# Optimization experiments

Measured on AMD Instinct MI355X. Metric: run time of the kernel, lower is better.

## Reference

```python
import jax, jax.numpy as jnp
import numpy as np

B, T, E, K, NNEG = 128, 512, 128, 4, 64


def setup_inputs() -> dict:
    key = jax.random.key(0)
    k1, k2, k3, k4 = jax.random.split(key, 4)
    base_payload = jax.random.normal(k1, (B, T, E), dtype=jnp.float32)
    mapped_ctx_payload = jax.random.normal(k2, (B, T, E, K), dtype=jnp.float32)
    seq_lens = jax.random.randint(k3, (B,), 1, T + 1, dtype=jnp.int32)
    # valid positions mask over the flattened (B*T) pool of possible negatives
    valid = (jnp.arange(T)[None, :] < seq_lens[:, None]).reshape(-1)  # [B*T]
    logits = jnp.where(valid, 0.0, -1e30)[None, :]                    # [1, B*T]
    logits = jnp.broadcast_to(logits, (B, B * T))
    # mirrors torch.multinomial(mask, n_negatives): one draw set per batch row
    sample_ids = jax.random.categorical(k4, logits, shape=(NNEG, B)).T.astype(jnp.int32)
    return {
        "base_payload": base_payload,
        "mapped_ctx_payload": mapped_ctx_payload,
        "seq_lens": seq_lens,
        "sample_ids": sample_ids,
    }


def reference(base_payload, mapped_ctx_payload, seq_lens, sample_ids):
    b, t, e = base_payload.shape
    n_steps = mapped_ctx_payload.shape[-1]
    # length mask [b, t]
    len_mask = (jnp.arange(t)[None, :] < seq_lens[:, None]).astype(base_payload.dtype)
    # zero context embeddings past each sequence's length
    trimmed_mce = mapped_ctx_payload * len_mask[:, :, None, None]  # [b, t, e, n_steps]
    # gather sampled negatives from the flattened base embedding pool
    neg_samples = base_payload.reshape(b * t, e)[sample_ids]  # [b, n_neg, e]

    step_losses = []
    for i in range(1, n_steps + 1):
        ce_i = trimmed_mce[:, : t - i, :, i - 1]   # [b, t-i, e]
        be_i = base_payload[:, i:]                  # [b, t-i, e]
        positive_pred = jnp.sum(ce_i * be_i, axis=-1)             # [b, t-i]
        neg_pred = jnp.einsum('bse,bne->bsn', ce_i, neg_samples)  # [b, t-i, n_neg]
        logits = jnp.concatenate([positive_pred[..., None], neg_pred], axis=-1)
        step_losses.append(-jax.nn.log_softmax(logits, axis=-1)[:, :, 0].mean())
    return jnp.stack(step_losses).mean()
```

## Files before the change

kernel.cpp:

```cpp
#include <hip/hip_runtime.h>
#include <math.h>

#define NB 128
#define NT 512
#define NEDIM 128
#define NNEG 64
#define SCHUNK 16
#define NCHUNK (NT / SCHUNK)
#define NBLK (NB * NCHUNK)
#define WSN (NBLK * 4)

typedef __bf16 bf16x8 __attribute__((ext_vector_type(8)));
typedef float  f32x4  __attribute__((ext_vector_type(4)));

__launch_bounds__(256, 4)
__global__ void cpc_mfma_kernel(const float* __restrict__ base,
                                const float* __restrict__ mce,
                                const int*  __restrict__ seq_lens,
                                const int*  __restrict__ sample_ids,
                                float* __restrict__ ws)
{
    const int b    = blockIdx.y;
    const int s0   = blockIdx.x * SCHUNK;
    const int slot = (b * NCHUNK + blockIdx.x) * 4;
    const int L    = seq_lens[b];
    const float LOG65 = 4.1743873f;
    const float wgt[4] = {1.f/261632.f, 1.f/261120.f, 1.f/260608.f, 1.f/260096.f};

    if (s0 >= L) {
        if (threadIdx.x < 4) {
            float c = 0.f;
            #pragma unroll
            for (int i = 1; i <= 4; ++i) {
                int hi = min(SCHUNK, (NT - i) - s0);
                if (hi > 0) c += (float)hi * LOG65 * wgt[i - 1];
            }
            ws[slot + threadIdx.x] = (threadIdx.x == 0) ? c : 0.f;
        }
        return;
    }

    __shared__ __bf16 Afrag[1024 * 8];
    __shared__ __bf16 Bfrag[1536 * 8];

    const int tid  = threadIdx.x;
    const int lane = tid & 63;
    const int w    = tid >> 6;
    const int q    = lane >> 4;
    const int fl   = lane & 15;

    const float4* mce4 = (const float4*)mce;

    {
        int s  = tid & 15;
        int eb = tid >> 4;
        const float4* src = mce4 + (size_t)(b * NT + s0 + s) * NEDIM + eb * 8;
        float4 v[8];
        #pragma unroll
        for (int u = 0; u < 8; ++u) v[u] = src[u];
        const float* vf = (const float*)v;
        int Cs = (eb >> 2) * 4 + (s >> 2);
        int base_chunk = Cs * 64 + (eb & 3) * 16 + (s & 3) * 4;
        int x = Cs & 7;
        #pragma unroll
        for (int k = 0; k < 4; ++k) {
            int phys = (base_chunk + k) ^ x;
            bf16x8 o;
            #pragma unroll
            for (int u = 0; u < 8; ++u) o[u] = (__bf16)vf[4 * u + k];
            *(bf16x8*)(&Afrag[phys * 8]) = o;
        }
    }

    #pragma unroll
    for (int it = 0; it < 4; ++it) {
        int h  = tid + 256 * it;
        int n  = h >> 4;
        int eb = h & 15;
        int r  = sample_ids[b * NNEG + n];
        const float4* srcb = (const float4*)(base + (size_t)r * NEDIM);
        float4 v0 = srcb[eb * 2], v1 = srcb[eb * 2 + 1];
        const float* f0 = (const float*)&v0;
        const float* f1 = (const float*)&v1;
        bf16x8 o;
        #pragma unroll
        for (int u = 0; u < 4; ++u) { o[u] = (__bf16)f0[u]; o[4 + u] = (__bf16)f1[u]; }
        int phys = (eb * 96 + n) ^ (eb & 7);
        *(bf16x8*)(&Bfrag[phys * 8]) = o;
    }

    #pragma unroll
    for (int it = 0; it < 2; ++it) {
        int h  = tid + 256 * it;
        int j  = h >> 4;
        int eb = h & 15;
        bf16x8 o;
        #pragma unroll
        for (int u = 0; u < 8; ++u) o[u] = (__bf16)0.f;
        if (j < SCHUNK + 3) {
            int srow = s0 + 1 + j; if (srow > NT - 1) srow = NT - 1;
            const float4* srcp = (const float4*)(base + (size_t)(b * NT + srow) * NEDIM);
            float4 v0 = srcp[eb * 2], v1 = srcp[eb * 2 + 1];
            const float* f0 = (const float*)&v0;
            const float* f1 = (const float*)&v1;
            #pragma unroll
            for (int u = 0; u < 4; ++u) { o[u] = (__bf16)f0[u]; o[4 + u] = (__bf16)f1[u]; }
        }
        int phys = (eb * 96 + 64 + j) ^ (eb & 7);
        *(bf16x8*)(&Bfrag[phys * 8]) = o;
    }
    __syncthreads();

    f32x4 acc[6];
    #pragma unroll
    for (int nt = 0; nt < 6; ++nt) acc[nt] = (f32x4){0.f, 0.f, 0.f, 0.f};

    #pragma unroll
    for (int kstep = 0; kstep < 4; ++kstep) {
        int CsA = kstep * 4 + w;
        bf16x8 af = *(const bf16x8*)(&Afrag[((CsA * 64 + lane) ^ (CsA & 7)) * 8]);
        int ebB = kstep * 4 + q;
        int xb  = ebB & 7;
        bf16x8 bv[6];
        #pragma unroll
        for (int nt = 0; nt < 6; ++nt)
            bv[nt] = *(const bf16x8*)(&Bfrag[((ebB * 96 + nt * 16 + fl) ^ xb) * 8]);
        #pragma unroll
        for (int nt = 0; nt < 6; ++nt)
            acc[nt] = __builtin_amdgcn_mfma_f32_16x16x32_bf16(af, bv[nt], acc[nt], 0, 0, 0);
    }

    const int sloc = w * 4 + q;
    const int sg   = s0 + sloc;
    float lossacc = 0.f;
    #pragma unroll
    for (int r = 0; r < 4; ++r) {
        int ip   = r + 1;
        int pcol = sloc + r;
        float z0 = acc[0][r], z1 = acc[1][r];
        float z2 = acc[2][r], z3 = acc[3][r];
        float pv = (pcol < 16) ? acc[4][r] : acc[5][r];
        float p  = __shfl(pv, (lane & 48) | (pcol & 15));
        float mx = fmaxf(fmaxf(z0, z1), fmaxf(z2, z3));
        mx = fmaxf(mx, __shfl_xor(mx, 1));
        mx = fmaxf(mx, __shfl_xor(mx, 2));
        mx = fmaxf(mx, __shfl_xor(mx, 4));
        mx = fmaxf(mx, __shfl_xor(mx, 8));
        mx = fmaxf(mx, p);
        float es = __expf(z0 - mx) + __expf(z1 - mx)
                 + __expf(z2 - mx) + __expf(z3 - mx);
        es += __shfl_xor(es, 1);
        es += __shfl_xor(es, 2);
        es += __shfl_xor(es, 4);
        es += __shfl_xor(es, 8);
        es += __expf(p - mx);
        float loss = __logf(es) + (mx - p);
        loss = (sg < L) ? loss : LOG65;
        bool take = (sg < NT - ip) && (fl == 0);
        lossacc += take ? wgt[r] * loss : 0.f;
    }
    lossacc += __shfl_xor(lossacc, 16);
    lossacc += __shfl_xor(lossacc, 32);
    if (lane == 0) ws[slot + w] = lossacc;
}

__global__ void reduce_k(const float* __restrict__ ws, float* __restrict__ out) {
    const int tid = threadIdx.x;
    float s = 0.f;
    #pragma unroll
    for (int i = 0; i < WSN / 256; ++i) s += ws[tid + 256 * i];
    s += __shfl_xor(s, 1);
    s += __shfl_xor(s, 2);
    s += __shfl_xor(s, 4);
    s += __shfl_xor(s, 8);
    s += __shfl_xor(s, 16);
    s += __shfl_xor(s, 32);
    __shared__ float wsum[4];
    if ((tid & 63) == 0) wsum[tid >> 6] = s;
    __syncthreads();
    if (tid == 0) out[0] = wsum[0] + wsum[1] + wsum[2] + wsum[3];
}

extern "C" void kernel_launch(void* const* d_in, const int* in_sizes, int n_in,
                              void* d_out, int out_size, void* d_ws, size_t ws_size,
                              hipStream_t stream) {
    (void)in_sizes; (void)n_in; (void)out_size; (void)ws_size;
    const float* base       = (const float*)d_in[0];
    const float* mce        = (const float*)d_in[1];
    const int*   seq_lens   = (const int*)d_in[2];
    const int*   sample_ids = (const int*)d_in[3];
    float* out = (float*)d_out;
    float* ws  = (float*)d_ws;

    dim3 grid(NCHUNK, NB);
    cpc_mfma_kernel<<<grid, 256, 0, stream>>>(base, mce, seq_lens, sample_ids, ws);
    reduce_k<<<1, 256, 0, stream>>>(ws, out);
}
```

Measured before the change: 211.9 us.

## Pre-pack negative samples to bf16 once per batch and DMA into LDS

Adds a small pre-kernel that gathers the 64 sampled negative rows per batch, converts them to bf16 and stores them in workspace in fragment order. The main kernel then copies them straight into shared memory with global_load_lds, replacing the per-block gather and conversion that every one of the 32 chunks repeated. The positive rows move to a separate LDS buffer. The aim is to cut redundant gathers and conversion work, at the cost of an extra launch and workspace traffic.

```diff
diff --git a/kernel.cpp b/kernel.cpp
--- a/kernel.cpp
+++ b/kernel.cpp
@@ -9,15 +9,46 @@
 #define NCHUNK (NT / SCHUNK)
 #define NBLK (NB * NCHUNK)
 #define WSN (NBLK * 4)
+#define NEG_OFF 65536
 
 typedef __bf16 bf16x8 __attribute__((ext_vector_type(8)));
 typedef float  f32x4  __attribute__((ext_vector_type(4)));
+
+#define GAS(p) ((const __attribute__((address_space(1))) void*)(p))
+#define LAS(p) ((__attribute__((address_space(3))) void*)(p))
+
+__device__ __forceinline__ bf16x8 pack8(float4 v0, float4 v1) {
+    const float* f0 = (const float*)&v0;
+    const float* f1 = (const float*)&v1;
+    bf16x8 o;
+    #pragma unroll
+    for (int u = 0; u < 4; ++u) { o[u] = (__bf16)f0[u]; o[4 + u] = (__bf16)f1[u]; }
+    return o;
+}
+
+__global__ void neg_pack_kernel(const float* __restrict__ base,
+                                const int*  __restrict__ sample_ids,
+                                __bf16* __restrict__ negbuf)
+{
+    const int b   = blockIdx.x;
+    const int tid = threadIdx.x;
+    const int n   = tid & 63;
+    const int r   = sample_ids[b * NNEG + n];
+    const float4* src = (const float4*)(base + (size_t)r * NEDIM);
+    __bf16* dstb = negbuf + (size_t)b * 1024 * 8;
+    #pragma unroll
+    for (int it = 0; it < 4; ++it) {
+        int eb = (tid >> 6) + 4 * it;
+        float4 v0 = src[eb * 2], v1 = src[eb * 2 + 1];
+        *(bf16x8*)(dstb + (size_t)(eb * 64 + n) * 8) = pack8(v0, v1);
+    }
+}
 
 __launch_bounds__(256, 4)
 __global__ void cpc_mfma_kernel(const float* __restrict__ base,
                                 const float* __restrict__ mce,
                                 const int*  __restrict__ seq_lens,
-                                const int*  __restrict__ sample_ids,
+                                const __bf16* __restrict__ negbuf,
                                 float* __restrict__ ws)
 {
     const int b    = blockIdx.y;
@@ -40,8 +71,9 @@
         return;
     }
 
-    __shared__ __bf16 Afrag[1024 * 8];
-    __shared__ __bf16 Bfrag[1536 * 8];
+    __shared__ __align__(16) __bf16 Afrag[1024 * 8];
+    __shared__ __align__(16) __bf16 Bfrag[1024 * 8];
+    __shared__ __align__(16) __bf16 Pfrag[512 * 8];
 
     const int tid  = threadIdx.x;
     const int lane = tid & 63;
@@ -49,7 +81,28 @@
     const int q    = lane >> 4;
     const int fl   = lane & 15;
 
+    {
+        const __bf16* negb = negbuf + (size_t)b * 1024 * 8;
+        #pragma unroll
+        for (int ebi = 0; ebi < 4; ++ebi) {
+            int eb = w * 4 + ebi;
+            int x  = eb & 7;
+            const __bf16* src = negb + (size_t)(eb * 64 + (lane ^ x)) * 8;
+            __builtin_amdgcn_global_load_lds(GAS(src), LAS(&Bfrag[eb * 64 * 8]), 16, 0, 0);
+        }
+    }
+
     const float4* mce4 = (const float4*)mce;
+    #pragma unroll
+    for (int it = 0; it < 2; ++it) {
+        int h  = tid + 256 * it;
+        int j  = h >> 4;
+        int eb = h & 15;
+        int srow = s0 + 1 + j; if (srow > NT - 1) srow = NT - 1;
+        const float4* srcp = (const float4*)(base + (size_t)(b * NT + srow) * NEDIM) + eb * 2;
+        float4 v0 = srcp[0], v1 = srcp[1];
+        *(bf16x8*)(&Pfrag[(size_t)((eb * 32 + j) ^ (eb & 7)) * 8]) = pack8(v0, v1);
+    }
 
     {
         int s  = tid & 15;
@@ -71,44 +124,6 @@
             *(bf16x8*)(&Afrag[phys * 8]) = o;
         }
     }
-
-    #pragma unroll
-    for (int it = 0; it < 4; ++it) {
-        int h  = tid + 256 * it;
-        int n  = h >> 4;
-        int eb = h & 15;
-        int r  = sample_ids[b * NNEG + n];
-        const float4* srcb = (const float4*)(base + (size_t)r * NEDIM);
-        float4 v0 = srcb[eb * 2], v1 = srcb[eb * 2 + 1];
-        const float* f0 = (const float*)&v0;
-        const float* f1 = (const float*)&v1;
-        bf16x8 o;
-        #pragma unroll
-        for (int u = 0; u < 4; ++u) { o[u] = (__bf16)f0[u]; o[4 + u] = (__bf16)f1[u]; }
-        int phys = (eb * 96 + n) ^ (eb & 7);
-        *(bf16x8*)(&Bfrag[phys * 8]) = o;
-    }
-
-    #pragma unroll
-    for (int it = 0; it < 2; ++it) {
-        int h  = tid + 256 * it;
-        int j  = h >> 4;
-        int eb = h & 15;
-        bf16x8 o;
-        #pragma unroll
-        for (int u = 0; u < 8; ++u) o[u] = (__bf16)0.f;
-        if (j < SCHUNK + 3) {
-            int srow = s0 + 1 + j; if (srow > NT - 1) srow = NT - 1;
-            const float4* srcp = (const float4*)(base + (size_t)(b * NT + srow) * NEDIM);
-            float4 v0 = srcp[eb * 2], v1 = srcp[eb * 2 + 1];
-            const float* f0 = (const float*)&v0;
-            const float* f1 = (const float*)&v1;
-            #pragma unroll
-            for (int u = 0; u < 4; ++u) { o[u] = (__bf16)f0[u]; o[4 + u] = (__bf16)f1[u]; }
-        }
-        int phys = (eb * 96 + 64 + j) ^ (eb & 7);
-        *(bf16x8*)(&Bfrag[phys * 8]) = o;
-    }
     __syncthreads();
 
     f32x4 acc[6];
@@ -123,8 +138,11 @@
         int xb  = ebB & 7;
         bf16x8 bv[6];
         #pragma unroll
-        for (int nt = 0; nt < 6; ++nt)
-            bv[nt] = *(const bf16x8*)(&Bfrag[((ebB * 96 + nt * 16 + fl) ^ xb) * 8]);
+        for (int nt = 0; nt < 4; ++nt)
+            bv[nt] = *(const bf16x8*)(&Bfrag[((ebB * 64 + nt * 16 + fl) ^ xb) * 8]);
+        #pragma unroll
+        for (int t = 0; t < 2; ++t)
+            bv[4 + t] = *(const bf16x8*)(&Pfrag[((ebB * 32 + t * 16 + fl) ^ xb) * 8]);
         #pragma unroll
         for (int nt = 0; nt < 6; ++nt)
             acc[nt] = __builtin_amdgcn_mfma_f32_16x16x32_bf16(af, bv[nt], acc[nt], 0, 0, 0);
@@ -191,8 +209,10 @@
     const int*   sample_ids = (const int*)d_in[3];
     float* out = (float*)d_out;
     float* ws  = (float*)d_ws;
-
+    __bf16* negbuf = (__bf16*)(ws + NEG_OFF);
+
+    neg_pack_kernel<<<dim3(NB), 256, 0, stream>>>(base, sample_ids, negbuf);
     dim3 grid(NCHUNK, NB);
-    cpc_mfma_kernel<<<grid, 256, 0, stream>>>(base, mce, seq_lens, sample_ids, ws);
+    cpc_mfma_kernel<<<grid, 256, 0, stream>>>(base, mce, seq_lens, negbuf, ws);
     reduce_k<<<1, 256, 0, stream>>>(ws, out);
 }
```

After: 214.7 us. No clear change (+1.3%).

## Load MFMA fragments directly from global memory, dropping LDS staging

Applied to the files above, without the earlier changes.

Removes the shared-memory staging of the context and negative/positive base tiles, along with the block barrier. Each lane now builds its bf16 MFMA operand fragments straight from global memory: it selects its step component from float4 loads of the context payload and packs gathered base rows. The aim is to cut LDS write/read traffic and the synchronisation stall. In exchange, each wave redundantly reloads the same base rows, and context loads fetch four floats to use one, which leans on cache hits.

```diff
diff --git a/kernel.cpp b/kernel.cpp
--- a/kernel.cpp
+++ b/kernel.cpp
@@ -12,6 +12,13 @@
 
 typedef __bf16 bf16x8 __attribute__((ext_vector_type(8)));
 typedef float  f32x4  __attribute__((ext_vector_type(4)));
+
+__device__ __forceinline__ bf16x8 pack8(float4 v0, float4 v1) {
+    bf16x8 o;
+    o[0] = (__bf16)v0.x; o[1] = (__bf16)v0.y; o[2] = (__bf16)v0.z; o[3] = (__bf16)v0.w;
+    o[4] = (__bf16)v1.x; o[5] = (__bf16)v1.y; o[6] = (__bf16)v1.z; o[7] = (__bf16)v1.w;
+    return o;
+}
 
 __launch_bounds__(256, 4)
 __global__ void cpc_mfma_kernel(const float* __restrict__ base,
@@ -40,76 +47,30 @@
         return;
     }
 
-    __shared__ __bf16 Afrag[1024 * 8];
-    __shared__ __bf16 Bfrag[1536 * 8];
-
     const int tid  = threadIdx.x;
     const int lane = tid & 63;
     const int w    = tid >> 6;
     const int q    = lane >> 4;
     const int fl   = lane & 15;
+    const int k    = fl & 3;
+    const bool c1  = (k & 1) != 0;
+    const bool c2  = (k & 2) != 0;
 
-    const float4* mce4 = (const float4*)mce;
+    const float4* arow4 = (const float4*)mce + (size_t)(b * NT + s0 + w * 4 + (fl >> 2)) * NEDIM;
 
-    {
-        int s  = tid & 15;
-        int eb = tid >> 4;
-        const float4* src = mce4 + (size_t)(b * NT + s0 + s) * NEDIM + eb * 8;
-        float4 v[8];
-        #pragma unroll
-        for (int u = 0; u < 8; ++u) v[u] = src[u];
-        const float* vf = (const float*)v;
-        int Cs = (eb >> 2) * 4 + (s >> 2);
-        int base_chunk = Cs * 64 + (eb & 3) * 16 + (s & 3) * 4;
-        int x = Cs & 7;
-        #pragma unroll
-        for (int k = 0; k < 4; ++k) {
-            int phys = (base_chunk + k) ^ x;
-            bf16x8 o;
-            #pragma unroll
-            for (int u = 0; u < 8; ++u) o[u] = (__bf16)vf[4 * u + k];
-            *(bf16x8*)(&Afrag[phys * 8]) = o;
-        }
+    const float4* base4 = (const float4*)base;
+    const float4* nrow[4];
+    #pragma unroll
+    for (int nt = 0; nt < 4; ++nt) {
+        int r = sample_ids[b * NNEG + nt * 16 + fl];
+        nrow[nt] = base4 + (size_t)r * (NEDIM / 4);
     }
-
+    const float4* prow[2];
     #pragma unroll
-    for (int it = 0; it < 4; ++it) {
-        int h  = tid + 256 * it;
-        int n  = h >> 4;
-        int eb = h & 15;
-        int r  = sample_ids[b * NNEG + n];
-        const float4* srcb = (const float4*)(base + (size_t)r * NEDIM);
-        float4 v0 = srcb[eb * 2], v1 = srcb[eb * 2 + 1];
-        const float* f0 = (const float*)&v0;
-        const float* f1 = (const float*)&v1;
-        bf16x8 o;
-        #pragma unroll
-        for (int u = 0; u < 4; ++u) { o[u] = (__bf16)f0[u]; o[4 + u] = (__bf16)f1[u]; }
-        int phys = (eb * 96 + n) ^ (eb & 7);
-        *(bf16x8*)(&Bfrag[phys * 8]) = o;
+    for (int t = 0; t < 2; ++t) {
+        int srow = s0 + 1 + t * 16 + fl; if (srow > NT - 1) srow = NT - 1;
+        prow[t] = base4 + (size_t)(b * NT + srow) * (NEDIM / 4);
     }
-
-    #pragma unroll
-    for (int it = 0; it < 2; ++it) {
-        int h  = tid + 256 * it;
-        int j  = h >> 4;
-        int eb = h & 15;
-        bf16x8 o;
-        #pragma unroll
-        for (int u = 0; u < 8; ++u) o[u] = (__bf16)0.f;
-        if (j < SCHUNK + 3) {
-            int srow = s0 + 1 + j; if (srow > NT - 1) srow = NT - 1;
-            const float4* srcp = (const float4*)(base + (size_t)(b * NT + srow) * NEDIM);
-            float4 v0 = srcp[eb * 2], v1 = srcp[eb * 2 + 1];
-            const float* f0 = (const float*)&v0;
-            const float* f1 = (const float*)&v1;
-            #pragma unroll
-            for (int u = 0; u < 4; ++u) { o[u] = (__bf16)f0[u]; o[4 + u] = (__bf16)f1[u]; }
-        }
-        int phys = (eb * 96 + 64 + j) ^ (eb & 7);
-        *(bf16x8*)(&Bfrag[phys * 8]) = o;
-    }
-    __syncthreads();
 
     f32x4 acc[6];
     #pragma unroll
@@ -117,14 +78,26 @@
 
     #pragma unroll
     for (int kstep = 0; kstep < 4; ++kstep) {
-        int CsA = kstep * 4 + w;
-        bf16x8 af = *(const bf16x8*)(&Afrag[((CsA * 64 + lane) ^ (CsA & 7)) * 8]);
-        int ebB = kstep * 4 + q;
-        int xb  = ebB & 7;
+        const int e0  = kstep * 32 + q * 8;
+        const int e04 = kstep * 8 + q * 2;
+
+        bf16x8 af;
+        #pragma unroll
+        for (int j = 0; j < 8; ++j) {
+            float4 f = arow4[e0 + j];
+            float lo = c1 ? f.y : f.x;
+            float hi = c1 ? f.w : f.z;
+            af[j] = (__bf16)(c2 ? hi : lo);
+        }
+
         bf16x8 bv[6];
         #pragma unroll
-        for (int nt = 0; nt < 6; ++nt)
-            bv[nt] = *(const bf16x8*)(&Bfrag[((ebB * 96 + nt * 16 + fl) ^ xb) * 8]);
+        for (int nt = 0; nt < 4; ++nt)
+            bv[nt] = pack8(nrow[nt][e04], nrow[nt][e04 + 1]);
+        #pragma unroll
+        for (int t = 0; t < 2; ++t)
+            bv[4 + t] = pack8(prow[t][e04], prow[t][e04 + 1]);
+
         #pragma unroll
         for (int nt = 0; nt < 6; ++nt)
             acc[nt] = __builtin_amdgcn_mfma_f32_16x16x32_bf16(af, bv[nt], acc[nt], 0, 0, 0);
```

Result: slower. 273.1 us (+28.9%).

## Process four sequence chunks per block with double-buffered prefetch and shared negatives

Applied to the files above, without the earlier changes.

Each block now handles four consecutive 16-row chunks instead of one. The 64 gathered negative-sample rows are loaded and converted to bf16 once per block and reused for all four chunks. The next chunk's context and positive rows are prefetched into registers while the current chunk's MFMA and softmax run, then written to a double-buffered shared-memory slot. This cuts redundant gathers and hides global load latency, at the cost of a 4x smaller grid, extra barriers per chunk, and the occupancy hint lowered from 4 to 2.

```diff
diff --git a/kernel.cpp b/kernel.cpp
--- a/kernel.cpp
+++ b/kernel.cpp
@@ -6,14 +6,35 @@
 #define NEDIM 128
 #define NNEG 64
 #define SCHUNK 16
-#define NCHUNK (NT / SCHUNK)
-#define NBLK (NB * NCHUNK)
-#define WSN (NBLK * 4)
+#define CPB 4
+#define SBLK (SCHUNK * CPB)
+#define NXBLK (NT / SBLK)
+#define NBLKS (NB * NXBLK)
+#define WSN (NBLKS * 4)
 
 typedef __bf16 bf16x8 __attribute__((ext_vector_type(8)));
 typedef float  f32x4  __attribute__((ext_vector_type(4)));
 
-__launch_bounds__(256, 4)
+__device__ __forceinline__ bf16x8 pack8(float4 v0, float4 v1) {
+    bf16x8 o;
+    o[0] = (__bf16)v0.x; o[1] = (__bf16)v0.y; o[2] = (__bf16)v0.z; o[3] = (__bf16)v0.w;
+    o[4] = (__bf16)v1.x; o[5] = (__bf16)v1.y; o[6] = (__bf16)v1.z; o[7] = (__bf16)v1.w;
+    return o;
+}
+
+__device__ __forceinline__ float chunk_const(int s0c) {
+    const float wgt[4] = {1.f/261632.f, 1.f/261120.f, 1.f/260608.f, 1.f/260096.f};
+    const float LOG65 = 4.1743873f;
+    float c = 0.f;
+    #pragma unroll
+    for (int i = 1; i <= 4; ++i) {
+        int hi = min(SCHUNK, (NT - i) - s0c);
+        if (hi > 0) c += (float)hi * LOG65 * wgt[i - 1];
+    }
+    return c;
+}
+
+__launch_bounds__(256, 2)
 __global__ void cpc_mfma_kernel(const float* __restrict__ base,
                                 const float* __restrict__ mce,
                                 const int*  __restrict__ seq_lens,
@@ -21,8 +42,8 @@
                                 float* __restrict__ ws)
 {
     const int b    = blockIdx.y;
-    const int s0   = blockIdx.x * SCHUNK;
-    const int slot = (b * NCHUNK + blockIdx.x) * 4;
+    const int s0   = blockIdx.x * SBLK;
+    const int slot = (b * NXBLK + blockIdx.x) * 4;
     const int L    = seq_lens[b];
     const float LOG65 = 4.1743873f;
     const float wgt[4] = {1.f/261632.f, 1.f/261120.f, 1.f/260608.f, 1.f/260096.f};
@@ -30,18 +51,18 @@
     if (s0 >= L) {
         if (threadIdx.x < 4) {
             float c = 0.f;
-            #pragma unroll
-            for (int i = 1; i <= 4; ++i) {
-                int hi = min(SCHUNK, (NT - i) - s0);
-                if (hi > 0) c += (float)hi * LOG65 * wgt[i - 1];
-            }
-            ws[slot + threadIdx.x] = (threadIdx.x == 0) ? c : 0.f;
+            if (threadIdx.x == 0) {
+                #pragma unroll
+                for (int cc = 0; cc < CPB; ++cc) c += chunk_const(s0 + cc * SCHUNK);
+            }
+            ws[slot + threadIdx.x] = c;
         }
         return;
     }
 
-    __shared__ __bf16 Afrag[1024 * 8];
-    __shared__ __bf16 Bfrag[1536 * 8];
+    __shared__ __align__(16) __bf16 Afrag[2][1024 * 8];
+    __shared__ __align__(16) __bf16 Bfrag[1024 * 8];
+    __shared__ __align__(16) __bf16 Pfrag[2][512 * 8];
 
     const int tid  = threadIdx.x;
     const int lane = tid & 63;
@@ -49,28 +70,8 @@
     const int q    = lane >> 4;
     const int fl   = lane & 15;
 
-    const float4* mce4 = (const float4*)mce;
-
-    {
-        int s  = tid & 15;
-        int eb = tid >> 4;
-        const float4* src = mce4 + (size_t)(b * NT + s0 + s) * NEDIM + eb * 8;
-        float4 v[8];
-        #pragma unroll
-        for (int u = 0; u < 8; ++u) v[u] = src[u];
-        const float* vf = (const float*)v;
-        int Cs = (eb >> 2) * 4 + (s >> 2);
-        int base_chunk = Cs * 64 + (eb & 3) * 16 + (s & 3) * 4;
-        int x = Cs & 7;
-        #pragma unroll
-        for (int k = 0; k < 4; ++k) {
-            int phys = (base_chunk + k) ^ x;
-            bf16x8 o;
-            #pragma unroll
-            for (int u = 0; u < 8; ++u) o[u] = (__bf16)vf[4 * u + k];
-            *(bf16x8*)(&Afrag[phys * 8]) = o;
-        }
-    }
+    const float4* mce4  = (const float4*)mce;
+    const float4* base4 = (const float4*)base;
 
     #pragma unroll
     for (int it = 0; it < 4; ++it) {
@@ -78,87 +79,152 @@
         int n  = h >> 4;
         int eb = h & 15;
         int r  = sample_ids[b * NNEG + n];
-        const float4* srcb = (const float4*)(base + (size_t)r * NEDIM);
-        float4 v0 = srcb[eb * 2], v1 = srcb[eb * 2 + 1];
-        const float* f0 = (const float*)&v0;
-        const float* f1 = (const float*)&v1;
-        bf16x8 o;
+        const float4* srcb = base4 + (size_t)r * (NEDIM / 4) + eb * 2;
+        float4 v0 = srcb[0], v1 = srcb[1];
+        *(bf16x8*)(&Bfrag[(size_t)((eb * 64 + n) ^ (eb & 7)) * 8]) = pack8(v0, v1);
+    }
+
+    const int sA  = tid & 15;
+    const int ebA = tid >> 4;
+    const int CsS = (ebA >> 2) * 4 + (sA >> 2);
+    const int bcA = CsS * 64 + (ebA & 3) * 16 + (sA & 3) * 4;
+    const int xA  = CsS & 7;
+
+    {
+        const float4* src = mce4 + (size_t)(b * NT + s0 + sA) * NEDIM + ebA * 8;
+        float4 v[8];
         #pragma unroll
-        for (int u = 0; u < 4; ++u) { o[u] = (__bf16)f0[u]; o[4 + u] = (__bf16)f1[u]; }
-        int phys = (eb * 96 + n) ^ (eb & 7);
-        *(bf16x8*)(&Bfrag[phys * 8]) = o;
-    }
-
-    #pragma unroll
-    for (int it = 0; it < 2; ++it) {
-        int h  = tid + 256 * it;
-        int j  = h >> 4;
-        int eb = h & 15;
-        bf16x8 o;
+        for (int u = 0; u < 8; ++u) v[u] = src[u];
+        const float* vf = (const float*)v;
         #pragma unroll
-        for (int u = 0; u < 8; ++u) o[u] = (__bf16)0.f;
-        if (j < SCHUNK + 3) {
+        for (int k = 0; k < 4; ++k) {
+            bf16x8 o;
+            #pragma unroll
+            for (int u = 0; u < 8; ++u) o[u] = (__bf16)vf[4 * u + k];
+            *(bf16x8*)(&Afrag[0][(size_t)((bcA + k) ^ xA) * 8]) = o;
+        }
+        #pragma unroll
+        for (int it = 0; it < 2; ++it) {
+            int h = tid + 256 * it;
+            int j = h >> 4, ebP = h & 15;
             int srow = s0 + 1 + j; if (srow > NT - 1) srow = NT - 1;
-            const float4* srcp = (const float4*)(base + (size_t)(b * NT + srow) * NEDIM);
-            float4 v0 = srcp[eb * 2], v1 = srcp[eb * 2 + 1];
-            const float* f0 = (const float*)&v0;
-            const float* f1 = (const float*)&v1;
-            #pragma unroll
-            for (int u = 0; u < 4; ++u) { o[u] = (__bf16)f0[u]; o[4 + u] = (__bf16)f1[u]; }
-        }
-        int phys = (eb * 96 + 64 + j) ^ (eb & 7);
-        *(bf16x8*)(&Bfrag[phys * 8]) = o;
+            const float4* srcp = base4 + (size_t)(b * NT + srow) * (NEDIM / 4) + ebP * 2;
+            *(bf16x8*)(&Pfrag[0][(size_t)((ebP * 32 + j) ^ (ebP & 7)) * 8]) = pack8(srcp[0], srcp[1]);
+        }
     }
     __syncthreads();
 
-    f32x4 acc[6];
-    #pragma unroll
-    for (int nt = 0; nt < 6; ++nt) acc[nt] = (f32x4){0.f, 0.f, 0.f, 0.f};
-
-    #pragma unroll
-    for (int kstep = 0; kstep < 4; ++kstep) {
-        int CsA = kstep * 4 + w;
-        bf16x8 af = *(const bf16x8*)(&Afrag[((CsA * 64 + lane) ^ (CsA & 7)) * 8]);
-        int ebB = kstep * 4 + q;
-        int xb  = ebB & 7;
-        bf16x8 bv[6];
-        #pragma unroll
-        for (int nt = 0; nt < 6; ++nt)
-            bv[nt] = *(const bf16x8*)(&Bfrag[((ebB * 96 + nt * 16 + fl) ^ xb) * 8]);
-        #pragma unroll
-        for (int nt = 0; nt < 6; ++nt)
-            acc[nt] = __builtin_amdgcn_mfma_f32_16x16x32_bf16(af, bv[nt], acc[nt], 0, 0, 0);
-    }
-
+    float lossacc = 0.f;
     const int sloc = w * 4 + q;
-    const int sg   = s0 + sloc;
-    float lossacc = 0.f;
-    #pragma unroll
-    for (int r = 0; r < 4; ++r) {
-        int ip   = r + 1;
-        int pcol = sloc + r;
-        float z0 = acc[0][r], z1 = acc[1][r];
-        float z2 = acc[2][r], z3 = acc[3][r];
-        float pv = (pcol < 16) ? acc[4][r] : acc[5][r];
-        float p  = __shfl(pv, (lane & 48) | (pcol & 15));
-        float mx = fmaxf(fmaxf(z0, z1), fmaxf(z2, z3));
-        mx = fmaxf(mx, __shfl_xor(mx, 1));
-        mx = fmaxf(mx, __shfl_xor(mx, 2));
-        mx = fmaxf(mx, __shfl_xor(mx, 4));
-        mx = fmaxf(mx, __shfl_xor(mx, 8));
-        mx = fmaxf(mx, p);
-        float es = __expf(z0 - mx) + __expf(z1 - mx)
-                 + __expf(z2 - mx) + __expf(z3 - mx);
-        es += __shfl_xor(es, 1);
-        es += __shfl_xor(es, 2);
-        es += __shfl_xor(es, 4);
-        es += __shfl_xor(es, 8);
-        es += __expf(p - mx);
-        float loss = __logf(es) + (mx - p);
-        loss = (sg < L) ? loss : LOG65;
-        bool take = (sg < NT - ip) && (fl == 0);
-        lossacc += take ? wgt[r] * loss : 0.f;
-    }
+
+    for (int c = 0; c < CPB; ++c) {
+        const int s0c = s0 + c * SCHUNK;
+        const bool vcur  = (s0c < L);
+        const bool vnext = (c + 1 < CPB) && (s0 + (c + 1) * SCHUNK < L);
+
+        float4 av[8];
+        float4 pv0a, pv0b, pv1a, pv1b;
+        if (vnext) {
+            const int s0n = s0c + SCHUNK;
+            const float4* src = mce4 + (size_t)(b * NT + s0n + sA) * NEDIM + ebA * 8;
+            #pragma unroll
+            for (int u = 0; u < 8; ++u) av[u] = src[u];
+            {
+                int j = tid >> 4, ebP = tid & 15;
+                int srow = s0n + 1 + j; if (srow > NT - 1) srow = NT - 1;
+                const float4* srcp = base4 + (size_t)(b * NT + srow) * (NEDIM / 4) + ebP * 2;
+                pv0a = srcp[0]; pv0b = srcp[1];
+            }
+            {
+                int h = tid + 256;
+                int j = h >> 4, ebP = h & 15;
+                int srow = s0n + 1 + j; if (srow > NT - 1) srow = NT - 1;
+                const float4* srcp = base4 + (size_t)(b * NT + srow) * (NEDIM / 4) + ebP * 2;
+                pv1a = srcp[0]; pv1b = srcp[1];
+            }
+        }
+
+        if (vcur) {
+            const __bf16* Ab = Afrag[c & 1];
+            const __bf16* Pb = Pfrag[c & 1];
+            f32x4 acc[6];
+            #pragma unroll
+            for (int nt = 0; nt < 6; ++nt) acc[nt] = (f32x4){0.f, 0.f, 0.f, 0.f};
+
+            #pragma unroll
+            for (int kstep = 0; kstep < 4; ++kstep) {
+                int CsA = kstep * 4 + w;
+                bf16x8 af = *(const bf16x8*)(&Ab[(size_t)(((CsA * 64 + lane) ^ (CsA & 7))) * 8]);
+                int ebB = kstep * 4 + q;
+                int xb  = ebB & 7;
+                bf16x8 bv[6];
+                #pragma unroll
+                for (int nt = 0; nt < 4; ++nt)
+                    bv[nt] = *(const bf16x8*)(&Bfrag[(size_t)(((ebB * 64 + nt * 16 + fl) ^ xb)) * 8]);
+                #pragma unroll
+                for (int t = 0; t < 2; ++t)
+                    bv[4 + t] = *(const bf16x8*)(&Pb[(size_t)(((ebB * 32 + t * 16 + fl) ^ xb)) * 8]);
+                #pragma unroll
+                for (int nt = 0; nt < 6; ++nt)
+                    acc[nt] = __builtin_amdgcn_mfma_f32_16x16x32_bf16(af, bv[nt], acc[nt], 0, 0, 0);
+            }
+
+            const int sg = s0c + sloc;
+            #pragma unroll
+            for (int r = 0; r < 4; ++r) {
+                int ip   = r + 1;
+                int pcol = sloc + r;
+                float z0 = acc[0][r], z1 = acc[1][r];
+                float z2 = acc[2][r], z3 = acc[3][r];
+                float pv = (pcol < 16) ? acc[4][r] : acc[5][r];
+                float p  = __shfl(pv, (lane & 48) | (pcol & 15));
+                float mx = fmaxf(fmaxf(z0, z1), fmaxf(z2, z3));
+                mx = fmaxf(mx, __shfl_xor(mx, 1));
+                mx = fmaxf(mx, __shfl_xor(mx, 2));
+                mx = fmaxf(mx, __shfl_xor(mx, 4));
+                mx = fmaxf(mx, __shfl_xor(mx, 8));
+                mx = fmaxf(mx, p);
+                float es = __expf(z0 - mx) + __expf(z1 - mx)
+                         + __expf(z2 - mx) + __expf(z3 - mx);
+                es += __shfl_xor(es, 1);
+                es += __shfl_xor(es, 2);
+                es += __shfl_xor(es, 4);
+                es += __shfl_xor(es, 8);
+                es += __expf(p - mx);
+                float loss = __logf(es) + (mx - p);
+                loss = (sg < L) ? loss : LOG65;
+                bool take = (sg < NT - ip) && (fl == 0);
+                lossacc += take ? wgt[r] * loss : 0.f;
+            }
+        } else if (tid == 0) {
+            lossacc += chunk_const(s0c);
+        }
+        __syncthreads();
+
+        if (vnext) {
+            __bf16* An = Afrag[(c + 1) & 1];
+            __bf16* Pn = Pfrag[(c + 1) & 1];
+            const float* vf = (const float*)av;
+            #pragma unroll
+            for (int k = 0; k < 4; ++k) {
+                bf16x8 o;
+                #pragma unroll
+                for (int u = 0; u < 8; ++u) o[u] = (__bf16)vf[4 * u + k];
+                *(bf16x8*)(&An[(size_t)((bcA + k) ^ xA) * 8]) = o;
+            }
+            {
+                int j = tid >> 4, ebP = tid & 15;
+                *(bf16x8*)(&Pn[(size_t)((ebP * 32 + j) ^ (ebP & 7)) * 8]) = pack8(pv0a, pv0b);
+            }
+            {
+                int h = tid + 256;
+                int j = h >> 4, ebP = h & 15;
+                *(bf16x8*)(&Pn[(size_t)((ebP * 32 + j) ^ (ebP & 7)) * 8]) = pack8(pv1a, pv1b);
+            }
+        }
+        __syncthreads();
+    }
+
     lossacc += __shfl_xor(lossacc, 16);
     lossacc += __shfl_xor(lossacc, 32);
     if (lane == 0) ws[slot + w] = lossacc;
@@ -192,7 +258,7 @@
     float* out = (float*)d_out;
     float* ws  = (float*)d_ws;
 
-    dim3 grid(NCHUNK, NB);
+    dim3 grid(NXBLK, NB);
     cpc_mfma_kernel<<<grid, 256, 0, stream>>>(base, mce, seq_lens, sample_ids, ws);
     reduce_k<<<1, 256, 0, stream>>>(ws, out);
 }
```

New measurement: 224.7 us. 1.06x slower.
